# Optimization experiments

Measured on AMD Instinct MI355X. Metric: run time of the kernel, lower is better.

Reference implementation:

```python
import jax, jax.numpy as jnp
import numpy as np
from jax import lax

B, C, N, COUT, H, W = 8, 64, 16, 3, 96, 96
EPS = 1e-5  # torch GroupNorm / InstanceNorm2d default eps


def group_norm(x, gamma, beta, groups):
    n, c, h, w = x.shape
    xg = x.reshape(n, groups, c // groups, h, w)
    mu = xg.mean((2, 3, 4), keepdims=True)
    var = xg.var((2, 3, 4), keepdims=True)
    xg = (xg - mu) / jnp.sqrt(var + EPS)
    return xg.reshape(n, c, h, w) * gamma[None, :, None, None] + beta[None, :, None, None]


def instance_norm(x, gamma, beta):
    mu = x.mean((2, 3), keepdims=True)
    var = x.var((2, 3), keepdims=True)
    return (x - mu) / jnp.sqrt(var + EPS) * gamma[None, :, None, None] + beta[None, :, None, None]


def conv3x3(x, w, b):
    y = lax.conv_general_dilated(x, w, (1, 1), 'SAME',
                                 dimension_numbers=('NCHW', 'OIHW', 'NCHW'))
    return y + b[None, :, None, None]


def setup_inputs() -> dict:
    key = jax.random.key(0)
    ks = jax.random.split(key, 8)
    p = {}
    p['sr'] = jax.random.normal(ks[0], (B, C, H, W), jnp.float32)
    p['tg'] = jax.random.normal(ks[1], (B, C, H, W), jnp.float32)
    # self.w : Conv2d(c, c*n, 1) -> 1x1 conv == matmul over channels
    p['w_w'] = jax.random.normal(ks[2], (C * N, C), jnp.float32) * 0.05
    p['w_b'] = jnp.zeros((C * N,), jnp.float32)
    # mask_block: GN(c//4,c), ReLU, Conv(c,64,3), GN(16,64), ReLU, Conv(64,1,3)
    p['gn1_g'] = jnp.ones((C,), jnp.float32)
    p['gn1_b'] = jnp.zeros((C,), jnp.float32)
    p['c1_w'] = jax.random.normal(ks[3], (64, C, 3, 3), jnp.float32) * 0.05
    p['c1_b'] = jnp.zeros((64,), jnp.float32)
    p['gn2_g'] = jnp.ones((64,), jnp.float32)
    p['gn2_b'] = jnp.zeros((64,), jnp.float32)
    p['c2_w'] = jax.random.normal(ks[4], (1, 64, 3, 3), jnp.float32) * 0.05
    p['c2_b'] = jnp.zeros((1,), jnp.float32)
    # gen_block: IN(n), ReLU, Conv(n,n,1), IN(n), ReLU, Conv(n,cout,1)
    p['in1_g'] = jnp.ones((N,), jnp.float32)
    p['in1_b'] = jnp.zeros((N,), jnp.float32)
    p['c3_w'] = jax.random.normal(ks[5], (N, N), jnp.float32) * 0.1
    p['c3_b'] = jnp.zeros((N,), jnp.float32)
    p['in2_g'] = jnp.ones((N,), jnp.float32)
    p['in2_b'] = jnp.zeros((N,), jnp.float32)
    p['c4_w'] = jax.random.normal(ks[6], (COUT, N), jnp.float32) * 0.1
    p['c4_b'] = jnp.zeros((COUT,), jnp.float32)
    return p


def reference(sr, tg, w_w, w_b, gn1_g, gn1_b, c1_w, c1_b, gn2_g, gn2_b,
              c2_w, c2_b, in1_g, in1_b, c3_w, c3_b, in2_g, in2_b, c4_w, c4_b):
    b, c, h, w = sr.shape
    n = N
    # 1x1 conv then view to capsule layout [b, n, c, h*w]
    s = jnp.einsum('oc,bchw->bohw', w_w, sr) + w_b[None, :, None, None]
    s = s.reshape(b, n, c, h * w)
    op = s.sum(3, keepdims=True)  # [b,n,c,1]
    cof = None
    for _ in range(3):  # fixed 3-step dynamic routing
        opn = op / jnp.maximum(jnp.linalg.norm(op, axis=2, keepdims=True), 1e-12)
        cof = jax.nn.softmax((s * opn).sum(2, keepdims=True), axis=3)  # [b,n,1,hw]
        op = (s * cof).sum(3, keepdims=True)  # [b,n,c,1]
    # broadcast capsule vectors onto target feature map
    msk_tg = (tg[:, None, :, :, :] + op[:, :, :, :, None]).reshape(b * n, c, h, w)
    x = group_norm(msk_tg, gn1_g, gn1_b, c // 4)
    x = conv3x3(jax.nn.relu(x), c1_w, c1_b)
    x = group_norm(x, gn2_g, gn2_b, 64 // 4)
    x = conv3x3(jax.nn.relu(x), c2_w, c2_b)  # [b*n,1,h,w]
    msk = x.reshape(b, n, h, w)
    # spatial center-of-mass loss
    hw_cof = jax.nn.softmax(msk.reshape(b, n, h * w), -1).reshape(b, n, h, w)[..., None]
    hw_idx = jnp.stack(jnp.meshgrid(jnp.linspace(-1.0, 1.0, h),
                                    jnp.linspace(-1.0, 1.0, w), indexing='ij'), -1)[None, None]
    hw_centr = (hw_cof * hw_idx).sum((2, 3), keepdims=True)  # [b,n,1,1,2]
    centr_loss = (hw_cof * (hw_idx - hw_centr) ** 2).sum((2, 3, 4)).mean()
    # gen_block + sigmoid activation
    g = instance_norm(msk, in1_g, in1_b)
    g = jnp.einsum('on,bnhw->bohw', c3_w, jax.nn.relu(g)) + c3_b[None, :, None, None]
    g = instance_norm(g, in2_g, in2_b)
    rec = jax.nn.sigmoid(jnp.einsum('on,bnhw->bohw', c4_w, jax.nn.relu(g)) + c4_b[None, :, None, None])
    # outer product capsule x mask: [b,n,c,1] x [b,n,h,w] -> [b,n,c,h,w]
    op_out = jnp.einsum('bnc,bnhw->bnchw', op[..., 0], msk)
    return (op_out, msk, rec, centr_loss, cof.reshape(b, n, h, w))
```

## Files before the change

### kernel.cpp

```cpp
#include <hip/hip_runtime.h>
#include <math.h>

#define BB 8
#define CC 64
#define NCAP 16
#define HH 96
#define WW 96
#define PP (HH*WW)
#define BNN (BB*NCAP)
#define EPSN 1e-5f

typedef short short8 __attribute__((ext_vector_type(8)));
typedef unsigned short u16x8 __attribute__((ext_vector_type(8)));
typedef unsigned short u16x4 __attribute__((ext_vector_type(4)));
typedef float float4v __attribute__((ext_vector_type(4)));

__device__ __forceinline__ float bf2f(unsigned short u){
  union{unsigned int i; float f;} x; x.i = ((unsigned int)u)<<16; return x.f;
}
__device__ __forceinline__ unsigned short f2bf(float f){
  union{float f; unsigned int i;} x; x.f=f;
  unsigned int r = x.i + 0x7fffu + ((x.i>>16)&1u);
  return (unsigned short)(r>>16);
}
__device__ __forceinline__ float4v mfma16(short8 a, short8 b, float4v c){
  return __builtin_amdgcn_mfma_f32_16x16x32_bf16(a, b, c, 0, 0, 0);
}

__device__ __forceinline__ float blkred_sum(float v, float* red4){
  int tid = threadIdx.x; int lane = tid & 63, wv = tid >> 6;
  #pragma unroll
  for (int off=32; off>0; off>>=1) v += __shfl_down(v, off, 64);
  __syncthreads();
  if (lane == 0) red4[wv] = v;
  __syncthreads();
  return red4[0] + red4[1] + red4[2] + red4[3];
}
__device__ __forceinline__ float blkred_max(float v, float* red4){
  int tid = threadIdx.x; int lane = tid & 63, wv = tid >> 6;
  #pragma unroll
  for (int off=32; off>0; off>>=1) v = fmaxf(v, __shfl_down(v, off, 64));
  __syncthreads();
  if (lane == 0) red4[wv] = v;
  __syncthreads();
  return fmaxf(fmaxf(red4[0], red4[1]), fmaxf(red4[2], red4[3]));
}

__global__ void kpre_tgt(const float* __restrict__ tg, unsigned short* __restrict__ tgt){
  int b = blockIdx.x/36, pc = blockIdx.x - (blockIdx.x/36)*36;
  int p = pc*256 + threadIdx.x;
  unsigned short vals[CC];
  #pragma unroll 8
  for (int c=0;c<CC;c++) vals[c] = f2bf(tg[((size_t)b*CC + c)*PP + p]);
  u16x8* dst = (u16x8*)&tgt[((size_t)b*PP + p)*CC];
  #pragma unroll
  for (int j=0;j<8;j++){
    u16x8 v;
    #pragma unroll
    for (int e=0;e<8;e++) v[e] = vals[j*8+e];
    dst[j] = v;
  }
}

__global__ void kw_bf16(const float* __restrict__ w1, unsigned short* __restrict__ Wt){
  int i = blockIdx.x*256 + threadIdx.x;
  int o = i/576; int rem = i - o*576; int c = rem/9; int tap = rem - c*9;
  Wt[(tap*CC + o)*CC + c] = f2bf(w1[i]);
}

__global__ void k0_colstats(const float* __restrict__ sr, const float* __restrict__ tg,
                            float* __restrict__ t, float* __restrict__ S1, float* __restrict__ S2){
  int row = blockIdx.x;
  const float* srp = sr + (size_t)row * PP;
  const float* tgp = tg + (size_t)row * PP;
  float s0=0.f, a1=0.f, a2=0.f;
  for (int p = threadIdx.x; p < PP; p += 256){
    s0 += srp[p];
    float v = tgp[p];
    a1 += v; a2 += v*v;
  }
  __shared__ float red4[4];
  s0 = blkred_sum(s0, red4);
  a1 = blkred_sum(a1, red4);
  a2 = blkred_sum(a2, red4);
  if (threadIdx.x == 0){ t[row]=s0; S1[row]=a1; S2[row]=a2; }
}

__global__ void k_update(const float* __restrict__ Wm, const float* __restrict__ wb,
                         const float* __restrict__ vec, float biasmul, int perB,
                         float* __restrict__ opv, float* __restrict__ uv, float* __restrict__ bu){
  int bn = blockIdx.x; int n = bn & (NCAP-1); int b = bn >> 4;
  int c = threadIdx.x;
  __shared__ float Wsh[CC*65];
  __shared__ float vsh[CC];
  __shared__ float opsh[CC];
  vsh[c] = perB ? vec[b*CC + c] : vec[bn*CC + c];
  const float* Wn = Wm + (size_t)n*CC*CC;
  for (int i=c;i<CC*CC;i+=64){ int r=i>>6, k=i&63; Wsh[r*65+k]=Wn[i]; }
  __syncthreads();
  float acc = biasmul * wb[n*CC + c];
  #pragma unroll 8
  for (int k=0;k<CC;k++) acc += Wsh[c*65+k]*vsh[k];
  opv[bn*CC+c] = acc;
  float ss = acc*acc;
  #pragma unroll
  for (int off=32;off>0;off>>=1) ss += __shfl_down(ss, off, 64);
  ss = __shfl(ss, 0, 64);
  float inv = 1.0f / fmaxf(sqrtf(ss), 1e-12f);
  opsh[c] = acc * inv;
  __syncthreads();
  float uacc = 0.f;
  #pragma unroll 8
  for (int k=0;k<CC;k++) uacc += opsh[k] * Wsh[k*65+c];
  uv[bn*CC+c] = uacc;
  float bb = opsh[c]*wb[n*CC+c];
  #pragma unroll
  for (int off=32;off>0;off>>=1) bb += __shfl_down(bb, off, 64);
  if (c==0) bu[bn] = bb;
}

__global__ __launch_bounds__(128) void k2f_dpass(
    const float* __restrict__ sr, const float* __restrict__ uv,
    const float* __restrict__ bu, float* __restrict__ dbuf,
    float* __restrict__ partm, float* __restrict__ partz,
    float* __restrict__ prt, int writed){
  int b = blockIdx.x / 72; int pc = blockIdx.x - b*72;
  int tid = threadIdx.x;
  int p = pc*128 + tid;
  __shared__ float ush[NCAP][CC];
  __shared__ float bush[NCAP];
  __shared__ float msh[NCAP];
  __shared__ float wsh[NCAP*132];
  __shared__ float srsh[CC*132];
  for (int i=tid;i<NCAP*CC;i+=128) ush[i>>6][i&63] = uv[b*NCAP*CC + i];
  if (tid < NCAP) bush[tid] = bu[b*NCAP+tid];
  __syncthreads();
  float acc[NCAP];
  #pragma unroll
  for (int n=0;n<NCAP;n++) acc[n]=bush[n];
  #pragma unroll 4
  for (int c=0;c<CC;c++){
    float v = sr[((size_t)b*CC + c)*PP + p];
    srsh[c*132+tid] = v;
    #pragma unroll
    for (int n=0;n<NCAP;n++) acc[n] += ush[n][c]*v;
  }
  #pragma unroll
  for (int n=0;n<NCAP;n++){
    wsh[n*132+tid] = acc[n];
    if (writed) dbuf[((size_t)(b*NCAP+n))*PP + p] = acc[n];
  }
  __syncthreads();
  {
    int n = tid >> 3, seg = tid & 7;
    float m = -1e30f;
    #pragma unroll
    for (int i=0;i<16;i++) m = fmaxf(m, wsh[n*132+seg*16+i]);
    #pragma unroll
    for (int off=1; off<8; off<<=1) m = fmaxf(m, __shfl_xor(m, off, 64));
    float z = 0.f;
    #pragma unroll
    for (int i=0;i<16;i++) z += __expf(wsh[n*132+seg*16+i] - m);
    #pragma unroll
    for (int off=1; off<8; off<<=1) z += __shfl_xor(z, off, 64);
    if (seg == 0){
      partm[(b*NCAP + n)*72 + pc] = m;
      partz[(b*NCAP + n)*72 + pc] = z;
      msh[n] = m;
    }
  }
  __syncthreads();
  #pragma unroll
  for (int n=0;n<NCAP;n++) wsh[n*132+tid] = __expf(wsh[n*132+tid]-msh[n]);
  __syncthreads();
  {
    int c = tid & 63, half = tid >> 6;
    float acc8[8];
    #pragma unroll
    for (int i=0;i<8;i++) acc8[i]=0.f;
    const float4* sp = (const float4*)&srsh[c*132];
    #pragma unroll 4
    for (int k=0;k<32;k++){
      float4 sv = sp[k];
      #pragma unroll
      for (int i=0;i<8;i++){
        float4 wv = *(const float4*)&wsh[(half*8+i)*132+4*k];
        acc8[i] += wv.x*sv.x + wv.y*sv.y + wv.z*sv.z + wv.w*sv.w;
      }
    }
    float* pb = prt + (((size_t)b*72+pc)*NCAP + half*8)*CC + c;
    #pragma unroll
    for (int i=0;i<8;i++) pb[(size_t)i*CC] = acc8[i];
  }
}

__global__ void k3b_combine(const float* __restrict__ partm, const float* __restrict__ partz,
                            float* __restrict__ mrow, float* __restrict__ zrow){
  int bn = blockIdx.x; int t = threadIdx.x;
  float m1 = partm[bn*72 + t];
  float m2 = (t < 8) ? partm[bn*72 + 64 + t] : -1e30f;
  float mm = fmaxf(m1, m2);
  #pragma unroll
  for (int off=32;off>0;off>>=1) mm = fmaxf(mm, __shfl_xor(mm, off, 64));
  float z = partz[bn*72 + t]*__expf(m1 - mm);
  if (t < 8) z += partz[bn*72 + 64 + t]*__expf(m2 - mm);
  #pragma unroll
  for (int off=32;off>0;off>>=1) z += __shfl_xor(z, off, 64);
  if (t==0){ mrow[bn]=mm; zrow[bn]=z; }
}

__global__ void k4c_combine(const float* __restrict__ prt, const float* __restrict__ partm,
                            const float* __restrict__ mrow, const float* __restrict__ zrow,
                            float* __restrict__ rv){
  int bn = blockIdx.x; int b = bn >> 4, n = bn & (NCAP-1);
  int c = threadIdx.x;
  float M = mrow[bn], invZ = 1.0f/zrow[bn];
  float s = 0.f;
  #pragma unroll 8
  for (int pc=0;pc<72;pc++){
    float w = __expf(partm[bn*72+pc] - M);
    s += prt[(((size_t)b*72+pc)*NCAP + n)*CC + c] * w;
  }
  rv[bn*CC+c] = s*invZ;
}

__global__ void k6_cofout(const float* __restrict__ dbuf, const float* __restrict__ mrow,
                          const float* __restrict__ zrow, float* __restrict__ cof){
  int bn = blockIdx.y;
  int p = blockIdx.x*256 + threadIdx.x;
  float m=mrow[bn], invz=1.0f/zrow[bn];
  cof[(size_t)bn*PP+p] = __expf(dbuf[(size_t)bn*PP+p]-m)*invz;
}

__global__ void k7_gn1(const float* __restrict__ S1, const float* __restrict__ S2,
                       const float* __restrict__ opv, const float* __restrict__ g1,
                       const float* __restrict__ b1, float* __restrict__ Aaff,
                       float* __restrict__ Daff, float* __restrict__ gn2s,
                       float* __restrict__ gn2q, float* __restrict__ in2s,
                       float* __restrict__ in2q){
  int bn = blockIdx.x; int b = bn >> 4;
  int c = threadIdx.x;
  __shared__ float e1[CC], e2[CC], mu[16], ri[16];
  float op = opv[bn*CC+c];
  float s1 = S1[b*CC+c], s2 = S2[b*CC+c];
  e1[c] = s1 + (float)PP*op;
  e2[c] = s2 + 2.0f*op*s1 + (float)PP*op*op;
  __syncthreads();
  if (c < 16){
    float m  = (e1[4*c]+e1[4*c+1]+e1[4*c+2]+e1[4*c+3])*(1.0f/(4.0f*PP));
    float qq = (e2[4*c]+e2[4*c+1]+e2[4*c+2]+e2[4*c+3])*(1.0f/(4.0f*PP));
    mu[c]=m; ri[c]=rsqrtf(qq-m*m+EPSN);
    gn2s[bn*16+c]=0.f; gn2q[bn*16+c]=0.f;
  }
  if (bn==0){ in2s[c]=0.f; in2s[CC+c]=0.f; in2q[c]=0.f; in2q[CC+c]=0.f; }
  __syncthreads();
  int g = c>>2;
  float A = ri[g]*g1[c];
  Aaff[bn*CC+c]=A;
  Daff[bn*CC+c]=(op-mu[g])*A + b1[c];
}

__global__ __launch_bounds__(256, 3) void k8_conv1_mfma(
    const unsigned short* __restrict__ tgt, const unsigned short* __restrict__ Wt,
    const float* __restrict__ c1b, const float* __restrict__ Aaff,
    const float* __restrict__ Daff, unsigned short* __restrict__ y1b,
    float* __restrict__ gn2s, float* __restrict__ gn2q){
  int blk = blockIdx.x;
  int bn = blk/36, tt = blk - bn*36;
  int ty = tt/3, tx = tt - ty*3;
  int y0 = ty*8, x0 = tx*32;
  int b = bn >> 4;
  int tid = threadIdx.x, w = tid>>6, lane = tid&63, quad = lane>>4, col16 = lane&15;

  __shared__ unsigned short xh[10*34*72];
  __shared__ float Ash[CC], Dsh[CC];
  if (tid < CC){ Ash[tid]=Aaff[bn*CC+tid]; Dsh[tid]=Daff[bn*CC+tid]; }
  __syncthreads();

  const unsigned short* tgb = tgt + (size_t)b*PP*CC;
  for (int task = tid; task < 2720; task += 256){
    int j = task & 7, pi = task >> 3;
    int row = pi/34, col = pi - row*34;
    int gy = y0 + row - 1, gx = x0 + col - 1;
    u16x8 ov;
    if ((unsigned)gy < (unsigned)HH && (unsigned)gx < (unsigned)WW){
      u16x8 iv = *(const u16x8*)(tgb + ((size_t)(gy*WW+gx))*CC + j*8);
      #pragma unroll
      for (int e=0;e<8;e++){
        float f = bf2f(iv[e]);
        f = fmaxf(Ash[j*8+e]*f + Dsh[j*8+e], 0.f);
        ov[e] = f2bf(f);
      }
    } else {
      #pragma unroll
      for (int e=0;e<8;e++) ov[e]=0;
    }
    *(u16x8*)&xh[(row*34+col)*72 + j*8] = ov;
  }
  __syncthreads();

  float4v acc[4][4];
  #pragma unroll
  for (int mt=0;mt<4;mt++)
    #pragma unroll
    for (int nt=0;nt<4;nt++)
      #pragma unroll
      for (int e=0;e<4;e++) acc[mt][nt][e]=0.f;

  const unsigned short* xb0 = &xh[((2*w + 1)*34 + 1 + col16)*72 + quad*8];
  const unsigned short* wbase = Wt + (size_t)(col16*CC + quad*8);

  short8 a_c[4], b_c[4];
  {
    const int toff0 = ((0/3 - 1)*34 + (0%3) - 1)*72;
    #pragma unroll
    for (int mt=0;mt<4;mt++) a_c[mt] = *(const short8*)(wbase + 0*4096 + mt*1024);
    #pragma unroll
    for (int nt=0;nt<4;nt++){
      int ri = nt>>1, h = nt&1;
      b_c[nt] = *(const short8*)(xb0 + toff0 + ri*2448 + h*1152);
    }
  }
  #pragma unroll
  for (int s=0; s<18; ++s){
    short8 a_n[4], b_n[4];
    if (s < 17){
      const int s1 = s+1, tap1 = s1>>1, ch1 = s1&1;
      const int toff1 = ((tap1/3 - 1)*34 + (tap1%3) - 1)*72;
      #pragma unroll
      for (int mt=0;mt<4;mt++)
        a_n[mt] = *(const short8*)(wbase + tap1*4096 + mt*1024 + ch1*32);
      #pragma unroll
      for (int nt=0;nt<4;nt++){
        int ri = nt>>1, h = nt&1;
        b_n[nt] = *(const short8*)(xb0 + toff1 + ri*2448 + h*1152 + ch1*32);
      }
    }
    #pragma unroll
    for (int mt=0;mt<4;mt++)
      #pragma unroll
      for (int nt=0;nt<4;nt++)
        acc[mt][nt] = mfma16(a_c[mt], b_c[nt], acc[mt][nt]);
    if (s < 17){
      #pragma unroll
      for (int i=0;i<4;i++){ a_c[i]=a_n[i]; b_c[i]=b_n[i]; }
    }
  }

  unsigned short* ybn = y1b + (size_t)bn*PP*CC;
  #pragma unroll
  for (int mt=0;mt<4;mt++){
    float gs=0.f, gq=0.f;
    #pragma unroll
    for (int nt=0;nt<4;nt++){
      int ri = nt>>1, h = nt&1;
      int y = y0 + 2*w + ri, x = x0 + h*16 + col16;
      u16x4 pv;
      #pragma unroll
      for (int e=0;e<4;e++){
        int o = mt*16 + quad*4 + e;
        float v = acc[mt][nt][e] + c1b[o];
        pv[e] = f2bf(v);
        gs += v; gq += v*v;
      }
      *(u16x4*)&ybn[(size_t)(y*WW + x)*CC + mt*16 + quad*4] = pv;
    }
    #pragma unroll
    for (int off=1; off<16; off<<=1){
      gs += __shfl_xor(gs, off, 64);
      gq += __shfl_xor(gq, off, 64);
    }
    if (col16==0){
      atomicAdd(&gn2s[bn*16 + mt*4 + quad], gs);
      atomicAdd(&gn2q[bn*16 + mt*4 + quad], gq);
    }
  }
}

__global__ void k9_gn2fin(const float* __restrict__ gn2s, const float* __restrict__ gn2q,
                          const float* __restrict__ g2c, const float* __restrict__ b2c,
                          float* __restrict__ A2, float* __restrict__ D2){
  int bn = blockIdx.x; int o = threadIdx.x;
  int g = o>>2;
  float m = gn2s[bn*16+g]*(1.0f/(4.0f*PP));
  float q = gn2q[bn*16+g]*(1.0f/(4.0f*PP));
  float ri = rsqrtf(q - m*m + EPSN);
  float A = ri * g2c[o];
  A2[bn*CC+o] = A;
  D2[bn*CC+o] = b2c[o] - m*A;
}

__global__ __launch_bounds__(256) void k10_conv2(
    const unsigned short* __restrict__ y1b, const float* __restrict__ w2,
    const float* __restrict__ b2, const float* __restrict__ A2,
    const float* __restrict__ D2, float* __restrict__ mskout){
  int blk=blockIdx.x; int bn=blk/36; int tt=blk-bn*36;
  int y0=(tt/3)*8, x0=(tt%3)*32;
  int tid=threadIdx.x;
  __shared__ unsigned short xh2[10*34*72];
  __shared__ float wsh2[CC*9];
  __shared__ float Ash[CC], Dsh[CC];
  for (int i=tid;i<CC*9;i+=256) wsh2[i]=w2[i];
  if (tid<CC){ Ash[tid]=A2[bn*CC+tid]; Dsh[tid]=D2[bn*CC+tid]; }

  const unsigned short* yb = y1b + (size_t)bn*PP*CC;
  for (int task=tid; task<2720; task+=256){
    int j = task & 7, pi = task >> 3;
    int row = pi/34, col = pi - row*34;
    int gy = y0 + row - 1, gx = x0 + col - 1;
    u16x8 iv;
    if ((unsigned)gy < (unsigned)HH && (unsigned)gx < (unsigned)WW){
      iv = *(const u16x8*)(yb + ((size_t)(gy*WW+gx))*CC + j*8);
    } else {
      #pragma unroll
      for (int e=0;e<8;e++) iv[e]=0;
    }
    *(u16x8*)&xh2[(row*34+col)*72 + j*8] = iv;
  }
  __syncthreads();

  int xi = tid&31, yi = tid>>5;
  float acc = 0.f;
  for (int t=0; t<9; ++t){
    int kh = t/3, kw = t - kh*3;
    int gy2 = y0 + yi + kh - 1, gx2 = x0 + xi + kw - 1;
    if ((unsigned)gy2 < (unsigned)HH && (unsigned)gx2 < (unsigned)WW){
      const unsigned short* px = &xh2[((yi+kh)*34 + xi+kw)*72];
      #pragma unroll
      for (int oct=0; oct<8; ++oct){
        u16x8 v = *(const u16x8*)(px + oct*8);
        #pragma unroll
        for (int e=0;e<8;e++){
          int c = oct*8 + e;
          float xv = fmaxf(Ash[c]*bf2f(v[e]) + Dsh[c], 0.f);
          acc += wsh2[c*9 + t] * xv;
        }
      }
    }
  }
  acc += b2[0];
  mskout[(size_t)bn*PP + (size_t)(y0+yi)*WW + (x0+xi)] = acc;
}

__global__ void k11_mskstats(const float* __restrict__ msk, const float* __restrict__ in1g,
                             const float* __restrict__ in1b, float* __restrict__ in1A,
                             float* __restrict__ in1D, float* __restrict__ lossbn){
  int bn = blockIdx.x; int n = bn & (NCAP-1);
  const float* mp = msk + (size_t)bn*PP;
  __shared__ float red4[4];
  float mx=-1e30f, s=0.f, q=0.f;
  for (int p=threadIdx.x;p<PP;p+=256){ float v=mp[p]; mx=fmaxf(mx,v); s+=v; q+=v*v; }
  mx = blkred_max(mx, red4);
  s  = blkred_sum(s, red4);
  q  = blkred_sum(q, red4);
  float z=0.f, sy=0.f, sx=0.f, syy=0.f, sxx=0.f;
  for (int p=threadIdx.x;p<PP;p+=256){
    float e = __expf(mp[p]-mx);
    int py = p/WW, px = p - py*WW;
    float iy = -1.0f + py*(2.0f/95.0f);
    float ix = -1.0f + px*(2.0f/95.0f);
    z+=e; sy+=e*iy; sx+=e*ix; syy+=e*iy*iy; sxx+=e*ix*ix;
  }
  z=blkred_sum(z,red4); sy=blkred_sum(sy,red4); sx=blkred_sum(sx,red4);
  syy=blkred_sum(syy,red4); sxx=blkred_sum(sxx,red4);
  if (threadIdx.x==0){
    float invz=1.0f/z;
    float ey=sy*invz, ex=sx*invz;
    lossbn[bn]=(syy*invz-ey*ey)+(sxx*invz-ex*ex);
    float mu=s*(1.0f/PP), var=q*(1.0f/PP)-mu*mu;
    float A=rsqrtf(var+EPSN)*in1g[n];
    in1A[bn]=A; in1D[bn]=in1b[n]-mu*A;
  }
}

__global__ void k12_loss(const float* __restrict__ lossbn, float* __restrict__ lossout){
  int tid=threadIdx.x;
  float v = lossbn[tid];
  #pragma unroll
  for (int off=32;off>0;off>>=1) v += __shfl_down(v,off,64);
  __shared__ float r2[2];
  if ((tid&63)==0) r2[tid>>6]=v;
  __syncthreads();
  if (tid==0) lossout[0] = (r2[0]+r2[1]) * (1.0f/128.0f);
}

__global__ void k13_gen1(const float* __restrict__ msk, const float* __restrict__ in1A,
                         const float* __restrict__ in1D, const float* __restrict__ c3w,
                         const float* __restrict__ c3b, float* __restrict__ g2,
                         float* __restrict__ in2s, float* __restrict__ in2q){
  int b = blockIdx.x/36; int pc = blockIdx.x - b*36;
  int p = pc*256+threadIdx.x;
  __shared__ float wsh[NCAP*NCAP];
  __shared__ float Ash[NCAP], Dsh[NCAP], bsh[NCAP];
  if (threadIdx.x < NCAP*NCAP) wsh[threadIdx.x] = c3w[threadIdx.x];
  if (threadIdx.x < NCAP){
    Ash[threadIdx.x]=in1A[b*NCAP+threadIdx.x];
    Dsh[threadIdx.x]=in1D[b*NCAP+threadIdx.x];
    bsh[threadIdx.x]=c3b[threadIdx.x];
  }
  __syncthreads();
  float h[NCAP];
  #pragma unroll
  for (int n=0;n<NCAP;n++)
    h[n] = fmaxf(0.f, Ash[n]*msk[(size_t)(b*NCAP+n)*PP+p] + Dsh[n]);
  float g[NCAP];
  #pragma unroll
  for (int o=0;o<NCAP;o++){
    float a = bsh[o];
    #pragma unroll
    for (int n=0;n<NCAP;n++) a += wsh[o*NCAP+n]*h[n];
    g[o]=a;
    g2[(size_t)(b*NCAP+o)*PP+p]=a;
  }
  int lane = threadIdx.x & 63;
  #pragma unroll
  for (int o=0;o<NCAP;o++){
    float a=g[o], q=g[o]*g[o];
    #pragma unroll
    for (int off=32;off>0;off>>=1){ a+=__shfl_down(a,off,64); q+=__shfl_down(q,off,64); }
    if (lane==0){ atomicAdd(&in2s[b*NCAP+o],a); atomicAdd(&in2q[b*NCAP+o],q); }
  }
}

__global__ void k14_in2fin(const float* __restrict__ in2s, const float* __restrict__ in2q,
                           const float* __restrict__ g, const float* __restrict__ bb,
                           float* __restrict__ in2A, float* __restrict__ in2D){
  int i=threadIdx.x;
  int o=i&15;
  float m=in2s[i]*(1.0f/PP), q=in2q[i]*(1.0f/PP);
  float A=rsqrtf(q-m*m+EPSN)*g[o];
  in2A[i]=A; in2D[i]=bb[o]-m*A;
}

__global__ void k15_rec(const float* __restrict__ g2, const float* __restrict__ in2A,
                        const float* __restrict__ in2D, const float* __restrict__ c4w,
                        const float* __restrict__ c4b, float* __restrict__ rec){
  int b = blockIdx.x/36; int pc = blockIdx.x - b*36;
  int p = pc*256+threadIdx.x;
  __shared__ float wsh[3*NCAP], Ash[NCAP], Dsh[NCAP], bsh[3];
  if (threadIdx.x<3*NCAP) wsh[threadIdx.x]=c4w[threadIdx.x];
  if (threadIdx.x<NCAP){ Ash[threadIdx.x]=in2A[b*NCAP+threadIdx.x]; Dsh[threadIdx.x]=in2D[b*NCAP+threadIdx.x]; }
  if (threadIdx.x<3) bsh[threadIdx.x]=c4b[threadIdx.x];
  __syncthreads();
  float h[NCAP];
  #pragma unroll
  for (int o=0;o<NCAP;o++)
    h[o]=fmaxf(0.f, Ash[o]*g2[(size_t)(b*NCAP+o)*PP+p]+Dsh[o]);
  #pragma unroll
  for (int j=0;j<3;j++){
    float z=bsh[j];
    #pragma unroll
    for (int o=0;o<NCAP;o++) z += wsh[j*NCAP+o]*h[o];
    rec[(size_t)(b*3+j)*PP+p] = 1.0f/(1.0f+__expf(-z));
  }
}

__global__ void k16_opout(const float* __restrict__ opv, const float* __restrict__ msk,
                          float* __restrict__ out){
  int bn = blockIdx.x / 9; int pt = blockIdx.x - bn*9;
  int base = pt*1024;
  __shared__ float ms[1024];
  __shared__ float opl[CC];
  for (int i=threadIdx.x;i<1024;i+=256) ms[i]=msk[(size_t)bn*PP+base+i];
  if (threadIdx.x<CC) opl[threadIdx.x]=opv[bn*CC+threadIdx.x];
  __syncthreads();
  float4 mv = ((const float4*)ms)[threadIdx.x];
  float* obase = out + (size_t)bn*CC*PP + base;
  #pragma unroll 4
  for (int c=0;c<CC;c++){
    float ov = opl[c];
    ((float4*)(obase + (size_t)c*PP))[threadIdx.x] = make_float4(ov*mv.x,ov*mv.y,ov*mv.z,ov*mv.w);
  }
}

extern "C" void kernel_launch(void* const* d_in, const int* in_sizes, int n_in,
                              void* d_out, int out_size, void* d_ws, size_t ws_size,
                              hipStream_t stream){
  const float* sr   = (const float*)d_in[0];
  const float* tg   = (const float*)d_in[1];
  const float* w_w  = (const float*)d_in[2];
  const float* w_b  = (const float*)d_in[3];
  const float* gn1g = (const float*)d_in[4];
  const float* gn1b = (const float*)d_in[5];
  const float* c1w  = (const float*)d_in[6];
  const float* c1b  = (const float*)d_in[7];
  const float* gn2g = (const float*)d_in[8];
  const float* gn2b = (const float*)d_in[9];
  const float* c2w  = (const float*)d_in[10];
  const float* c2b  = (const float*)d_in[11];
  const float* in1g = (const float*)d_in[12];
  const float* in1b = (const float*)d_in[13];
  const float* c3w  = (const float*)d_in[14];
  const float* c3b  = (const float*)d_in[15];
  const float* in2g = (const float*)d_in[16];
  const float* in2b = (const float*)d_in[17];
  const float* c4w  = (const float*)d_in[18];
  const float* c4b  = (const float*)d_in[19];
  float* out = (float*)d_out;
  float* ws  = (float*)d_ws;

  float* t_   = ws + 0;
  float* S1   = ws + 512;
  float* S2   = ws + 1024;
  float* opv  = ws + 1536;
  float* uv   = ws + 9728;
  float* bu   = ws + 17920;
  float* mrow = ws + 18048;
  float* zrow = ws + 18176;
  float* rv   = ws + 18304;
  float* Aaff = ws + 26496;
  float* Daff = ws + 34688;
  float* gn2s = ws + 42880;
  float* gn2q = ws + 44928;
  float* A2   = ws + 46976;
  float* D2   = ws + 55168;
  float* in1A = ws + 63360;
  float* in1D = ws + 63488;
  float* lossbn = ws + 63616;
  float* in2s = ws + 63744;
  float* in2q = ws + 63872;
  float* in2A = ws + 64000;
  float* in2D = ws + 64128;
  float* dbuf = ws + 65536;
  float* g2   = ws + 65536 + 1179648;

  unsigned short* y1b = (unsigned short*)d_out;
  unsigned short* tgt = (unsigned short*)((char*)d_out + 150994944);
  unsigned short* Wt  = (unsigned short*)((char*)d_out + 160432128);
  float* prt   = (float*)((char*)d_out + 160505856);
  float* partm = (float*)((char*)d_out + 162865152);
  float* partz = (float*)((char*)d_out + 162902016);
  float* mskout  = out + 75497472;
  float* recout  = out + 76677120;
  float* lossout = out + 76898304;
  float* cofout  = out + 76898305;

  kpre_tgt<<<BB*36, 256, 0, stream>>>(tg, tgt);
  kw_bf16<<<144, 256, 0, stream>>>(c1w, Wt);
  k0_colstats<<<BB*CC, 256, 0, stream>>>(sr, tg, t_, S1, S2);
  k_update<<<BNN, 64, 0, stream>>>(w_w, w_b, t_, (float)PP, 1, opv, uv, bu);
  for (int it=0; it<3; ++it){
    k2f_dpass<<<BB*72, 128, 0, stream>>>(sr, uv, bu, dbuf, partm, partz, prt, it==2 ? 1 : 0);
    k3b_combine<<<BNN, 64, 0, stream>>>(partm, partz, mrow, zrow);
    k4c_combine<<<BNN, 64, 0, stream>>>(prt, partm, mrow, zrow, rv);
    k_update<<<BNN, 64, 0, stream>>>(w_w, w_b, rv, 1.0f, 0, opv, uv, bu);
  }
  k6_cofout<<<dim3(36, BNN), 256, 0, stream>>>(dbuf, mrow, zrow, cofout);
  k7_gn1<<<BNN, 64, 0, stream>>>(S1, S2, opv, gn1g, gn1b, Aaff, Daff, gn2s, gn2q, in2s, in2q);
  k8_conv1_mfma<<<BNN*36, 256, 0, stream>>>(tgt, Wt, c1b, Aaff, Daff, y1b, gn2s, gn2q);
  k9_gn2fin<<<BNN, 64, 0, stream>>>(gn2s, gn2q, gn2g, gn2b, A2, D2);
  k10_conv2<<<BNN*36, 256, 0, stream>>>(y1b, c2w, c2b, A2, D2, mskout);
  k11_mskstats<<<BNN, 256, 0, stream>>>(mskout, in1g, in1b, in1A, in1D, lossbn);
  k12_loss<<<1, 128, 0, stream>>>(lossbn, lossout);
  k13_gen1<<<BB*36, 256, 0, stream>>>(mskout, in1A, in1D, c3w, c3b, g2, in2s, in2q);
  k14_in2fin<<<1, 128, 0, stream>>>(in2s, in2q, in2g, in2b, in2A, in2D);
  k15_rec<<<BB*36, 256, 0, stream>>>(g2, in2A, in2D, c4w, c4b, recout);
  k16_opout<<<BNN*9, 256, 0, stream>>>(opv, mskout, out);
}
```

Measured before the change: 1.037 ms.

## Fuse small finalize kernels, merge routing iteration kernels, retile conv1 with staged stores

Merges the per-iteration softmax combine, weighted-sum and capsule update kernels into one kernel, and folds the GN2, IN2 and loss finalize kernels into their consumers, with the loss now accumulated by atomics. This removes several tiny launches per call. The conv1 MFMA kernel moves to 8x16 tiles with fewer accumulators and a higher occupancy target, and its bf16 output is staged through LDS so global stores are contiguous. The trade-offs are a larger halo-to-interior ratio in conv1 and redundant finalize math in every consumer block.

Measured after the change: 1.203 ms. 16.1% more time.

```diff
diff --git a/kernel.cpp b/kernel.cpp
--- a/kernel.cpp
+++ b/kernel.cpp
@@ -194,34 +194,57 @@
   }
 }
 
-__global__ void k3b_combine(const float* __restrict__ partm, const float* __restrict__ partz,
-                            float* __restrict__ mrow, float* __restrict__ zrow){
-  int bn = blockIdx.x; int t = threadIdx.x;
-  float m1 = partm[bn*72 + t];
-  float m2 = (t < 8) ? partm[bn*72 + 64 + t] : -1e30f;
+__global__ void k_iter(const float* __restrict__ prt, const float* __restrict__ partm,
+                       const float* __restrict__ partz, const float* __restrict__ Wm,
+                       const float* __restrict__ wb, float* __restrict__ mrow,
+                       float* __restrict__ zrow, float* __restrict__ opv,
+                       float* __restrict__ uv, float* __restrict__ bu){
+  int bn = blockIdx.x; int n = bn & (NCAP-1); int b = bn >> 4;
+  int c = threadIdx.x;
+  float m1 = partm[bn*72 + c];
+  float m2 = (c < 8) ? partm[bn*72 + 64 + c] : -1e30f;
   float mm = fmaxf(m1, m2);
   #pragma unroll
   for (int off=32;off>0;off>>=1) mm = fmaxf(mm, __shfl_xor(mm, off, 64));
-  float z = partz[bn*72 + t]*__expf(m1 - mm);
-  if (t < 8) z += partz[bn*72 + 64 + t]*__expf(m2 - mm);
+  float z = partz[bn*72 + c]*__expf(m1 - mm);
+  if (c < 8) z += partz[bn*72 + 64 + c]*__expf(m2 - mm);
   #pragma unroll
   for (int off=32;off>0;off>>=1) z += __shfl_xor(z, off, 64);
-  if (t==0){ mrow[bn]=mm; zrow[bn]=z; }
-}
-
-__global__ void k4c_combine(const float* __restrict__ prt, const float* __restrict__ partm,
-                            const float* __restrict__ mrow, const float* __restrict__ zrow,
-                            float* __restrict__ rv){
-  int bn = blockIdx.x; int b = bn >> 4, n = bn & (NCAP-1);
-  int c = threadIdx.x;
-  float M = mrow[bn], invZ = 1.0f/zrow[bn];
+  if (c==0){ mrow[bn]=mm; zrow[bn]=z; }
+  float invZ = 1.0f/z;
   float s = 0.f;
   #pragma unroll 8
   for (int pc=0;pc<72;pc++){
-    float w = __expf(partm[bn*72+pc] - M);
+    float w = __expf(partm[bn*72+pc] - mm);
     s += prt[(((size_t)b*72+pc)*NCAP + n)*CC + c] * w;
   }
-  rv[bn*CC+c] = s*invZ;
+  float rvc = s*invZ;
+  __shared__ float Wsh[CC*65];
+  __shared__ float vsh[CC];
+  __shared__ float opsh[CC];
+  vsh[c] = rvc;
+  const float* Wn = Wm + (size_t)n*CC*CC;
+  for (int i=c;i<CC*CC;i+=64){ int r=i>>6, k=i&63; Wsh[r*65+k]=Wn[i]; }
+  __syncthreads();
+  float acc = wb[n*CC + c];
+  #pragma unroll 8
+  for (int k=0;k<CC;k++) acc += Wsh[c*65+k]*vsh[k];
+  opv[bn*CC+c] = acc;
+  float ss = acc*acc;
+  #pragma unroll
+  for (int off=32;off>0;off>>=1) ss += __shfl_down(ss, off, 64);
+  ss = __shfl(ss, 0, 64);
+  float inv = 1.0f / fmaxf(sqrtf(ss), 1e-12f);
+  opsh[c] = acc * inv;
+  __syncthreads();
+  float uacc = 0.f;
+  #pragma unroll 8
+  for (int k=0;k<CC;k++) uacc += opsh[k] * Wsh[k*65+c];
+  uv[bn*CC+c] = uacc;
+  float bb = opsh[c]*wb[n*CC+c];
+  #pragma unroll
+  for (int off=32;off>0;off>>=1) bb += __shfl_down(bb, off, 64);
+  if (c==0) bu[bn] = bb;
 }
 
 __global__ void k6_cofout(const float* __restrict__ dbuf, const float* __restrict__ mrow,
@@ -237,7 +260,7 @@
                        const float* __restrict__ b1, float* __restrict__ Aaff,
                        float* __restrict__ Daff, float* __restrict__ gn2s,
                        float* __restrict__ gn2q, float* __restrict__ in2s,
-                       float* __restrict__ in2q){
+                       float* __restrict__ in2q, float* __restrict__ lossout){
   int bn = blockIdx.x; int b = bn >> 4;
   int c = threadIdx.x;
   __shared__ float e1[CC], e2[CC], mu[16], ri[16];
@@ -252,7 +275,10 @@
     mu[c]=m; ri[c]=rsqrtf(qq-m*m+EPSN);
     gn2s[bn*16+c]=0.f; gn2q[bn*16+c]=0.f;
   }
-  if (bn==0){ in2s[c]=0.f; in2s[CC+c]=0.f; in2q[c]=0.f; in2q[CC+c]=0.f; }
+  if (bn==0){
+    in2s[c]=0.f; in2s[CC+c]=0.f; in2q[c]=0.f; in2q[CC+c]=0.f;
+    if (c==0) lossout[0]=0.f;
+  }
   __syncthreads();
   int g = c>>2;
   float A = ri[g]*g1[c];
@@ -260,27 +286,27 @@
   Daff[bn*CC+c]=(op-mu[g])*A + b1[c];
 }
 
-__global__ __launch_bounds__(256, 3) void k8_conv1_mfma(
+__global__ __launch_bounds__(256, 6) void k8_conv1_mfma(
     const unsigned short* __restrict__ tgt, const unsigned short* __restrict__ Wt,
     const float* __restrict__ c1b, const float* __restrict__ Aaff,
     const float* __restrict__ Daff, unsigned short* __restrict__ y1b,
     float* __restrict__ gn2s, float* __restrict__ gn2q){
   int blk = blockIdx.x;
-  int bn = blk/36, tt = blk - bn*36;
-  int ty = tt/3, tx = tt - ty*3;
-  int y0 = ty*8, x0 = tx*32;
+  int bn = blk/72, tt = blk - bn*72;
+  int ty = tt/6, tx = tt - ty*6;
+  int y0 = ty*8, x0 = tx*16;
   int b = bn >> 4;
   int tid = threadIdx.x, w = tid>>6, lane = tid&63, quad = lane>>4, col16 = lane&15;
 
-  __shared__ unsigned short xh[10*34*72];
+  __shared__ unsigned short xh[10*18*72];
   __shared__ float Ash[CC], Dsh[CC];
   if (tid < CC){ Ash[tid]=Aaff[bn*CC+tid]; Dsh[tid]=Daff[bn*CC+tid]; }
   __syncthreads();
 
   const unsigned short* tgb = tgt + (size_t)b*PP*CC;
-  for (int task = tid; task < 2720; task += 256){
+  for (int task = tid; task < 1440; task += 256){
     int j = task & 7, pi = task >> 3;
-    int row = pi/34, col = pi - row*34;
+    int row = pi/18, col = pi - row*18;
     int gy = y0 + row - 1, gx = x0 + col - 1;
     u16x8 ov;
     if ((unsigned)gy < (unsigned)HH && (unsigned)gx < (unsigned)WW){
@@ -295,75 +321,58 @@
       #pragma unroll
       for (int e=0;e<8;e++) ov[e]=0;
     }
-    *(u16x8*)&xh[(row*34+col)*72 + j*8] = ov;
-  }
-  __syncthreads();
-
-  float4v acc[4][4];
+    *(u16x8*)&xh[(row*18+col)*72 + j*8] = ov;
+  }
+  __syncthreads();
+
+  float4v acc[4][2];
   #pragma unroll
   for (int mt=0;mt<4;mt++)
     #pragma unroll
-    for (int nt=0;nt<4;nt++)
-      #pragma unroll
-      for (int e=0;e<4;e++) acc[mt][nt][e]=0.f;
-
-  const unsigned short* xb0 = &xh[((2*w + 1)*34 + 1 + col16)*72 + quad*8];
+    for (int ri=0;ri<2;ri++)
+      #pragma unroll
+      for (int e=0;e<4;e++) acc[mt][ri][e]=0.f;
+
+  const unsigned short* xb0 = &xh[((2*w)*18 + col16)*72 + quad*8];
   const unsigned short* wbase = Wt + (size_t)(col16*CC + quad*8);
-
-  short8 a_c[4], b_c[4];
-  {
-    const int toff0 = ((0/3 - 1)*34 + (0%3) - 1)*72;
-    #pragma unroll
-    for (int mt=0;mt<4;mt++) a_c[mt] = *(const short8*)(wbase + 0*4096 + mt*1024);
-    #pragma unroll
-    for (int nt=0;nt<4;nt++){
-      int ri = nt>>1, h = nt&1;
-      b_c[nt] = *(const short8*)(xb0 + toff0 + ri*2448 + h*1152);
-    }
-  }
-  #pragma unroll
-  for (int s=0; s<18; ++s){
-    short8 a_n[4], b_n[4];
-    if (s < 17){
-      const int s1 = s+1, tap1 = s1>>1, ch1 = s1&1;
-      const int toff1 = ((tap1/3 - 1)*34 + (tap1%3) - 1)*72;
+  #pragma unroll
+  for (int tap=0; tap<9; ++tap){
+    const int dy = tap/3, dx = tap - (tap/3)*3;
+    const int toff = (dy*18 + dx)*72;
+    #pragma unroll
+    for (int chunk=0; chunk<2; ++chunk){
+      short8 a[4];
       #pragma unroll
       for (int mt=0;mt<4;mt++)
-        a_n[mt] = *(const short8*)(wbase + tap1*4096 + mt*1024 + ch1*32);
-      #pragma unroll
-      for (int nt=0;nt<4;nt++){
-        int ri = nt>>1, h = nt&1;
-        b_n[nt] = *(const short8*)(xb0 + toff1 + ri*2448 + h*1152 + ch1*32);
-      }
-    }
-    #pragma unroll
-    for (int mt=0;mt<4;mt++)
-      #pragma unroll
-      for (int nt=0;nt<4;nt++)
-        acc[mt][nt] = mfma16(a_c[mt], b_c[nt], acc[mt][nt]);
-    if (s < 17){
-      #pragma unroll
-      for (int i=0;i<4;i++){ a_c[i]=a_n[i]; b_c[i]=b_n[i]; }
-    }
-  }
-
-  unsigned short* ybn = y1b + (size_t)bn*PP*CC;
+        a[mt] = *(const short8*)(wbase + tap*4096 + mt*1024 + chunk*32);
+      short8 bf[2];
+      #pragma unroll
+      for (int ri=0;ri<2;ri++)
+        bf[ri] = *(const short8*)(xb0 + toff + ri*(18*72) + chunk*32);
+      #pragma unroll
+      for (int mt=0;mt<4;mt++)
+        #pragma unroll
+        for (int ri=0;ri<2;ri++)
+          acc[mt][ri] = mfma16(a[mt], bf[ri], acc[mt][ri]);
+    }
+  }
+
+  __syncthreads();
+  unsigned short* ybuf = xh;
   #pragma unroll
   for (int mt=0;mt<4;mt++){
     float gs=0.f, gq=0.f;
     #pragma unroll
-    for (int nt=0;nt<4;nt++){
-      int ri = nt>>1, h = nt&1;
-      int y = y0 + 2*w + ri, x = x0 + h*16 + col16;
+    for (int ri=0;ri<2;ri++){
       u16x4 pv;
       #pragma unroll
       for (int e=0;e<4;e++){
         int o = mt*16 + quad*4 + e;
-        float v = acc[mt][nt][e] + c1b[o];
+        float v = acc[mt][ri][e] + c1b[o];
         pv[e] = f2bf(v);
         gs += v; gq += v*v;
       }
-      *(u16x4*)&ybn[(size_t)(y*WW + x)*CC + mt*16 + quad*4] = pv;
+      *(u16x4*)&ybuf[((2*w+ri)*16 + col16)*72 + mt*16 + quad*4] = pv;
     }
     #pragma unroll
     for (int off=1; off<16; off<<=1){
@@ -375,33 +384,41 @@
       atomicAdd(&gn2q[bn*16 + mt*4 + quad], gq);
     }
   }
-}
-
-__global__ void k9_gn2fin(const float* __restrict__ gn2s, const float* __restrict__ gn2q,
-                          const float* __restrict__ g2c, const float* __restrict__ b2c,
-                          float* __restrict__ A2, float* __restrict__ D2){
-  int bn = blockIdx.x; int o = threadIdx.x;
-  int g = o>>2;
-  float m = gn2s[bn*16+g]*(1.0f/(4.0f*PP));
-  float q = gn2q[bn*16+g]*(1.0f/(4.0f*PP));
-  float ri = rsqrtf(q - m*m + EPSN);
-  float A = ri * g2c[o];
-  A2[bn*CC+o] = A;
-  D2[bn*CC+o] = b2c[o] - m*A;
+  __syncthreads();
+  unsigned short* ybn = y1b + (size_t)bn*PP*CC;
+  #pragma unroll
+  for (int pass=0; pass<4; ++pass){
+    int row = pass*2 + (tid>>7);
+    int chunk = tid & 127;
+    int pix = row*16 + (chunk>>3), c8 = chunk&7;
+    u16x8 v = *(const u16x8*)&ybuf[pix*72 + c8*8];
+    *(u16x8*)&ybn[(size_t)((y0+row)*WW + x0)*CC + chunk*8] = v;
+  }
 }
 
 __global__ __launch_bounds__(256) void k10_conv2(
     const unsigned short* __restrict__ y1b, const float* __restrict__ w2,
-    const float* __restrict__ b2, const float* __restrict__ A2,
-    const float* __restrict__ D2, float* __restrict__ mskout){
+    const float* __restrict__ b2, const float* __restrict__ gn2s,
+    const float* __restrict__ gn2q, const float* __restrict__ g2c,
+    const float* __restrict__ b2c, float* __restrict__ mskout){
   int blk=blockIdx.x; int bn=blk/36; int tt=blk-bn*36;
   int y0=(tt/3)*8, x0=(tt%3)*32;
   int tid=threadIdx.x;
   __shared__ unsigned short xh2[10*34*72];
   __shared__ float wsh2[CC*9];
   __shared__ float Ash[CC], Dsh[CC];
+  __shared__ float mg[16], rg[16];
   for (int i=tid;i<CC*9;i+=256) wsh2[i]=w2[i];
-  if (tid<CC){ Ash[tid]=A2[bn*CC+tid]; Dsh[tid]=D2[bn*CC+tid]; }
+  if (tid<16){
+    float m = gn2s[bn*16+tid]*(1.0f/(4.0f*PP));
+    float q = gn2q[bn*16+tid]*(1.0f/(4.0f*PP));
+    mg[tid]=m; rg[tid]=rsqrtf(q-m*m+EPSN);
+  }
+  __syncthreads();
+  if (tid<CC){
+    float A = rg[tid>>2]*g2c[tid];
+    Ash[tid]=A; Dsh[tid]=b2c[tid]-mg[tid>>2]*A;
+  }
 
   const unsigned short* yb = y1b + (size_t)bn*PP*CC;
   for (int task=tid; task<2720; task+=256){
@@ -444,7 +461,7 @@
 
 __global__ void k11_mskstats(const float* __restrict__ msk, const float* __restrict__ in1g,
                              const float* __restrict__ in1b, float* __restrict__ in1A,
-                             float* __restrict__ in1D, float* __restrict__ lossbn){
+                             float* __restrict__ in1D, float* __restrict__ lossout){
   int bn = blockIdx.x; int n = bn & (NCAP-1);
   const float* mp = msk + (size_t)bn*PP;
   __shared__ float red4[4];
@@ -466,22 +483,12 @@
   if (threadIdx.x==0){
     float invz=1.0f/z;
     float ey=sy*invz, ex=sx*invz;
-    lossbn[bn]=(syy*invz-ey*ey)+(sxx*invz-ex*ex);
+    float lv=(syy*invz-ey*ey)+(sxx*invz-ex*ex);
+    atomicAdd(lossout, lv*(1.0f/128.0f));
     float mu=s*(1.0f/PP), var=q*(1.0f/PP)-mu*mu;
     float A=rsqrtf(var+EPSN)*in1g[n];
     in1A[bn]=A; in1D[bn]=in1b[n]-mu*A;
   }
-}
-
-__global__ void k12_loss(const float* __restrict__ lossbn, float* __restrict__ lossout){
-  int tid=threadIdx.x;
-  float v = lossbn[tid];
-  #pragma unroll
-  for (int off=32;off>0;off>>=1) v += __shfl_down(v,off,64);
-  __shared__ float r2[2];
-  if ((tid&63)==0) r2[tid>>6]=v;
-  __syncthreads();
-  if (tid==0) lossout[0] = (r2[0]+r2[1]) * (1.0f/128.0f);
 }
 
 __global__ void k13_gen1(const float* __restrict__ msk, const float* __restrict__ in1A,
@@ -522,24 +529,20 @@
   }
 }
 
-__global__ void k14_in2fin(const float* __restrict__ in2s, const float* __restrict__ in2q,
-                           const float* __restrict__ g, const float* __restrict__ bb,
-                           float* __restrict__ in2A, float* __restrict__ in2D){
-  int i=threadIdx.x;
-  int o=i&15;
-  float m=in2s[i]*(1.0f/PP), q=in2q[i]*(1.0f/PP);
-  float A=rsqrtf(q-m*m+EPSN)*g[o];
-  in2A[i]=A; in2D[i]=bb[o]-m*A;
-}
-
-__global__ void k15_rec(const float* __restrict__ g2, const float* __restrict__ in2A,
-                        const float* __restrict__ in2D, const float* __restrict__ c4w,
+__global__ void k15_rec(const float* __restrict__ g2, const float* __restrict__ in2s,
+                        const float* __restrict__ in2q, const float* __restrict__ in2g,
+                        const float* __restrict__ in2b, const float* __restrict__ c4w,
                         const float* __restrict__ c4b, float* __restrict__ rec){
   int b = blockIdx.x/36; int pc = blockIdx.x - b*36;
   int p = pc*256+threadIdx.x;
   __shared__ float wsh[3*NCAP], Ash[NCAP], Dsh[NCAP], bsh[3];
   if (threadIdx.x<3*NCAP) wsh[threadIdx.x]=c4w[threadIdx.x];
-  if (threadIdx.x<NCAP){ Ash[threadIdx.x]=in2A[b*NCAP+threadIdx.x]; Dsh[threadIdx.x]=in2D[b*NCAP+threadIdx.x]; }
+  if (threadIdx.x<NCAP){
+    float m=in2s[b*NCAP+threadIdx.x]*(1.0f/PP);
+    float q=in2q[b*NCAP+threadIdx.x]*(1.0f/PP);
+    float A=rsqrtf(q-m*m+EPSN)*in2g[threadIdx.x];
+    Ash[threadIdx.x]=A; Dsh[threadIdx.x]=in2b[threadIdx.x]-m*A;
+  }
   if (threadIdx.x<3) bsh[threadIdx.x]=c4b[threadIdx.x];
   __syncthreads();
   float h[NCAP];
@@ -607,20 +610,14 @@
   float* bu   = ws + 17920;
   float* mrow = ws + 18048;
   float* zrow = ws + 18176;
-  float* rv   = ws + 18304;
   float* Aaff = ws + 26496;
   float* Daff = ws + 34688;
   float* gn2s = ws + 42880;
   float* gn2q = ws + 44928;
-  float* A2   = ws + 46976;
-  float* D2   = ws + 55168;
   float* in1A = ws + 63360;
   float* in1D = ws + 63488;
-  float* lossbn = ws + 63616;
   float* in2s = ws + 63744;
   float* in2q = ws + 63872;
-  float* in2A = ws + 64000;
-  float* in2D = ws + 64128;
   float* dbuf = ws + 65536;
   float* g2   = ws + 65536 + 1179648;
 
@@ -641,19 +638,14 @@
   k_update<<<BNN, 64, 0, stream>>>(w_w, w_b, t_, (float)PP, 1, opv, uv, bu);
   for (int it=0; it<3; ++it){
     k2f_dpass<<<BB*72, 128, 0, stream>>>(sr, uv, bu, dbuf, partm, partz, prt, it==2 ? 1 : 0);
-    k3b_combine<<<BNN, 64, 0, stream>>>(partm, partz, mrow, zrow);
-    k4c_combine<<<BNN, 64, 0, stream>>>(prt, partm, mrow, zrow, rv);
-    k_update<<<BNN, 64, 0, stream>>>(w_w, w_b, rv, 1.0f, 0, opv, uv, bu);
+    k_iter<<<BNN, 64, 0, stream>>>(prt, partm, partz, w_w, w_b, mrow, zrow, opv, uv, bu);
   }
   k6_cofout<<<dim3(36, BNN), 256, 0, stream>>>(dbuf, mrow, zrow, cofout);
-  k7_gn1<<<BNN, 64, 0, stream>>>(S1, S2, opv, gn1g, gn1b, Aaff, Daff, gn2s, gn2q, in2s, in2q);
-  k8_conv1_mfma<<<BNN*36, 256, 0, stream>>>(tgt, Wt, c1b, Aaff, Daff, y1b, gn2s, gn2q);
-  k9_gn2fin<<<BNN, 64, 0, stream>>>(gn2s, gn2q, gn2g, gn2b, A2, D2);
-  k10_conv2<<<BNN*36, 256, 0, stream>>>(y1b, c2w, c2b, A2, D2, mskout);
-  k11_mskstats<<<BNN, 256, 0, stream>>>(mskout, in1g, in1b, in1A, in1D, lossbn);
-  k12_loss<<<1, 128, 0, stream>>>(lossbn, lossout);
+  k7_gn1<<<BNN, 64, 0, stream>>>(S1, S2, opv, gn1g, gn1b, Aaff, Daff, gn2s, gn2q, in2s, in2q, lossout);
+  k8_conv1_mfma<<<BNN*72, 256, 0, stream>>>(tgt, Wt, c1b, Aaff, Daff, y1b, gn2s, gn2q);
+  k10_conv2<<<BNN*36, 256, 0, stream>>>(y1b, c2w, c2b, gn2s, gn2q, gn2g, gn2b, mskout);
+  k11_mskstats<<<BNN, 256, 0, stream>>>(mskout, in1g, in1b, in1A, in1D, lossout);
   k13_gen1<<<BB*36, 256, 0, stream>>>(mskout, in1A, in1D, c3w, c3b, g2, in2s, in2q);
-  k14_in2fin<<<1, 128, 0, stream>>>(in2s, in2q, in2g, in2b, in2A, in2D);
-  k15_rec<<<BB*36, 256, 0, stream>>>(g2, in2A, in2D, c4w, c4b, recout);
+  k15_rec<<<BB*36, 256, 0, stream>>>(g2, in2s, in2q, in2g, in2b, c4w, c4b, recout);
   k16_opout<<<BNN*9, 256, 0, stream>>>(opv, mskout, out);
 }
```
